# Kernel optimization log

Measured on AMD Instinct MI355X. Metric: run time of the kernel, lower is better.

Reference implementation:

```python
import jax, jax.numpy as jnp
import numpy as np

DIM = 1024
INTER = 4096
NUM_EXPERTS = 8
TOP_K = 2
NUM_TOKENS = 8192


def setup_inputs() -> dict:
    key = jax.random.key(0)
    ks = jax.random.split(key, 6)
    scale = 0.02
    return {
        "hidden_states": jax.random.normal(ks[0], (NUM_TOKENS, DIM), dtype=jnp.float32),
        # shared expert (stored as [in, out] so y = x @ W; same math as torch Linear)
        "shared_w1": jax.random.normal(ks[1], (DIM, INTER), dtype=jnp.float32) * scale,
        "shared_w2": jax.random.normal(ks[2], (INTER, DIM), dtype=jnp.float32) * scale,
        # routed experts, stacked: [E, in, out]
        "routed_w1": jax.random.normal(ks[3], (NUM_EXPERTS, DIM, INTER), dtype=jnp.float32) * scale,
        "routed_w2": jax.random.normal(ks[4], (NUM_EXPERTS, INTER, DIM), dtype=jnp.float32) * scale,
        # router: [dim, E]
        "router_w": jax.random.normal(ks[5], (DIM, NUM_EXPERTS), dtype=jnp.float32) * scale,
    }


def reference(hidden_states, shared_w1, shared_w2, routed_w1, routed_w2, router_w):
    # shared expert FFN
    shared_out = jnp.maximum(hidden_states @ shared_w1, 0) @ shared_w2  # [T, D]

    # router -> top-k -> softmax over the selected logits
    router_logits = hidden_states @ router_w                      # [T, E]
    top_vals, top_idx = jax.lax.top_k(router_logits, TOP_K)       # [T, K]
    routing_weights = jax.nn.softmax(top_vals, axis=-1)           # [T, K]

    # per-token combine weight for each expert: [T, E]
    onehot = jax.nn.one_hot(top_idx, NUM_EXPERTS, dtype=hidden_states.dtype)  # [T, K, E]
    combine = jnp.einsum('tk,tke->te', routing_weights, onehot)   # [T, E]

    # dense all-expert FFN (same math as gather/scatter loop, vectorized)
    h = jnp.einsum('td,edf->etf', hidden_states, routed_w1)       # [E, T, F]
    h = jnp.maximum(h, 0)
    expert_out = jnp.einsum('etf,efd->etd', h, routed_w2)         # [E, T, D]
    routed_out = jnp.einsum('etd,te->td', expert_out, combine)    # [T, D]

    return shared_out + routed_out
```

## Files before the change

### kernel.cpp

```cpp
#include <hip/hip_runtime.h>
#include <hip/hip_bf16.h>


#define T_TOKENS 8192
#define DIM      1024
#define INTER    4096
#define NEXP     8

typedef short bf16x8 __attribute__((ext_vector_type(8)));
typedef float f32x4  __attribute__((ext_vector_type(4)));

#define ASM_VMCNT(n) asm volatile("s_waitcnt vmcnt(" #n ")" ::: "memory")
#define ASM_BAR()    asm volatile("s_barrier" ::: "memory")

__device__ __forceinline__ unsigned short f2b(float f) {
  union { float f; unsigned int u; } v; v.f = f;
  unsigned int u = v.u;
  return (unsigned short)((u + 0x7FFFu + ((u >> 16) & 1u)) >> 16);
}

__device__ __forceinline__ void load_lds16(const unsigned short* g, unsigned short* l) {
  __builtin_amdgcn_global_load_lds(
      (const __attribute__((address_space(1))) void*)g,
      (__attribute__((address_space(3))) void*)l, 16, 0, 0);
}

__global__ void cast_x_kernel(const float* __restrict__ x, unsigned short* __restrict__ xb) {
  size_t i = ((size_t)blockIdx.x * 256 + threadIdx.x) * 4;
  float4 v = *(const float4*)(x + i);
  ushort4 o;
  o.x = f2b(v.x); o.y = f2b(v.y); o.z = f2b(v.z); o.w = f2b(v.w);
  *(ushort4*)(xb + i) = o;
}

__global__ void transpose_cast_kernel(const float* __restrict__ routed,
                                      const float* __restrict__ shared_w,
                                      unsigned short* __restrict__ outb,
                                      int K, int N) {
  int e = blockIdx.z;
  const float* in = (e < NEXP) ? routed + (size_t)e * K * N : shared_w;
  unsigned short* out = outb + (size_t)e * K * N;
  __shared__ float tile[32][33];
  int n0 = blockIdx.x * 32, k0 = blockIdx.y * 32;
  int tid = threadIdx.x;
  int c = tid & 31, r0 = tid >> 5;
#pragma unroll
  for (int i = 0; i < 4; i++) {
    int r = r0 + i * 8;
    tile[r][c] = in[(size_t)(k0 + r) * N + n0 + c];
  }
  __syncthreads();
  int rr = tid >> 3;
  int c4 = (tid & 7) * 4;
  ushort4 o;
  o.x = f2b(tile[c4 + 0][rr]); o.y = f2b(tile[c4 + 1][rr]);
  o.z = f2b(tile[c4 + 2][rr]); o.w = f2b(tile[c4 + 3][rr]);
  *(ushort4*)(out + (size_t)(n0 + rr) * K + k0 + c4) = o;
}

__global__ void router_topk_kernel(const float* __restrict__ x, const float* __restrict__ rw,
                                   int* __restrict__ top_idx, float* __restrict__ top_w) {
  int wv = threadIdx.x >> 6, lane = threadIdx.x & 63;
  int t = blockIdx.x * 4 + wv;
  const float* xr = x + (size_t)t * DIM;
  float a[8];
#pragma unroll
  for (int e = 0; e < 8; e++) a[e] = 0.f;
#pragma unroll
  for (int i = 0; i < 16; i++) {
    int d = i * 64 + lane;
    float xv = xr[d];
    float4 r0 = *(const float4*)(rw + d * 8);
    float4 r1 = *(const float4*)(rw + d * 8 + 4);
    a[0] += xv * r0.x; a[1] += xv * r0.y; a[2] += xv * r0.z; a[3] += xv * r0.w;
    a[4] += xv * r1.x; a[5] += xv * r1.y; a[6] += xv * r1.z; a[7] += xv * r1.w;
  }
#pragma unroll
  for (int s = 32; s; s >>= 1) {
#pragma unroll
    for (int e = 0; e < 8; e++) a[e] += __shfl_down(a[e], s);
  }
  if (lane == 0) {
    int be = 0; float bv = a[0];
#pragma unroll
    for (int e = 1; e < 8; e++) if (a[e] > bv) { bv = a[e]; be = e; }
    int be2 = -1; float bv2 = -3.4e38f;
#pragma unroll
    for (int e = 0; e < 8; e++) if (e != be && a[e] > bv2) { bv2 = a[e]; be2 = e; }
    float w0 = 1.f / (1.f + __expf(bv2 - bv));
    top_idx[t] = be | (be2 << 8);
    top_w[t] = w0;
  }
}

__global__ void bucket_kernel(const int* __restrict__ top_idx, const float* __restrict__ top_w,
                              int* __restrict__ counts, int* __restrict__ offs,
                              int* __restrict__ tok_list, float* __restrict__ tok_w) {
  __shared__ int lcount[NEXP];
  int tid = threadIdx.x;
  if (tid < NEXP) lcount[tid] = 0;
  __syncthreads();
  for (int t = tid; t < T_TOKENS; t += 256) {
    int p = top_idx[t];
    float w0 = top_w[t];
    int e0 = p & 0xff, e1 = p >> 8;
    int s0 = atomicAdd(&lcount[e0], 1);
    tok_list[e0 * T_TOKENS + s0] = t; tok_w[e0 * T_TOKENS + s0] = w0;
    int s1 = atomicAdd(&lcount[e1], 1);
    tok_list[e1 * T_TOKENS + s1] = t; tok_w[e1 * T_TOKENS + s1] = 1.f - w0;
  }
  __syncthreads();
  if (tid == 0) {
    int run = 0;
    for (int e = 0; e < NEXP; e++) { counts[e] = lcount[e]; offs[e] = run; run += lcount[e]; }
    offs[NEXP] = run;
  }
}

template <int PHASE>
__global__ __launch_bounds__(512, 2) void gemm_kernel(
    const unsigned short* __restrict__ A, const unsigned short* __restrict__ Wt,
    unsigned short* __restrict__ H, float* __restrict__ Out,
    const int* __restrict__ counts, const int* __restrict__ offs,
    const int* __restrict__ tok_list, const float* __restrict__ tok_w,
    int expert_arg, int accmode) {
  const int Kd = (PHASE == 1) ? DIM : INTER;
  int zz = (int)blockIdx.z;
  int expert, ksp;
  if (expert_arg >= 0) { expert = expert_arg; ksp = 0; }
  else if (PHASE == 2) { expert = zz % 9; ksp = zz / 9; }
  else { expert = zz; ksp = 0; }

  int count = (expert < NEXP) ? counts[expert] : T_TOKENS;
  int m0 = blockIdx.y * 256;
  if (m0 >= count) return;
  int n0 = blockIdx.x * 256;
  int hbase = (expert_arg >= 0) ? 0 : ((expert < NEXP) ? offs[expert] : 2 * T_TOKENS);
  const unsigned short* Bt = Wt + (size_t)expert * (4096 * 1024);

  int nt, k0base;
  if (PHASE == 1) { nt = 32; k0base = 0; }
  else if (expert_arg >= 0) { nt = 128; k0base = 0; }
  else { nt = 64; k0base = ksp * 2048; }

  __shared__ __align__(16) unsigned short As[4][256 * 32];
  __shared__ __align__(16) unsigned short Bs[4][256 * 32];

  int tid = threadIdx.x;
  int wv = tid >> 6, lane = tid & 63;
  int wv_m = wv >> 2, wv_n = wv & 3;
  int m_woff = wv_m * 128, n_woff = wv_n * 64;

  int g = (lane & 7) ^ (lane >> 3);
  int kc = (g & 3) * 8;
  const unsigned short* aG[2];
  const unsigned short* bG[2];
  int ldsOff[2];
#pragma unroll
  for (int j = 0; j < 2; j++) {
    int tr = j * 128 + wv * 16 + 2 * (lane >> 3) + (g >> 2);
    int srcA;
    if (PHASE == 1) {
      int m = m0 + tr;
      srcA = (expert < NEXP) ? ((m < count) ? tok_list[expert * T_TOKENS + m] : 0) : m;
    } else {
      srcA = hbase + m0 + tr;
    }
    aG[j] = A + (size_t)srcA * Kd + k0base + kc;
    bG[j] = Bt + (size_t)(n0 + tr) * Kd + k0base + kc;
    ldsOff[j] = j * 4096 + wv * 512;
  }

  f32x4 acc[8][4];
#pragma unroll
  for (int mf = 0; mf < 8; mf++)
#pragma unroll
    for (int nf = 0; nf < 4; nf++) acc[mf][nf] = (f32x4)0.f;

  int l15 = lane & 15, q = lane >> 4;
  int slot = (((l15 & 1) << 2) | q) ^ (l15 >> 1);
  int aBase = (wv_m * 64 + (l15 >> 1)) * 64 + slot * 8;
  int bBase = (wv_n * 32 + (l15 >> 1)) * 64 + slot * 8;

  auto stage = [&](int buf) {
#pragma unroll
    for (int j = 0; j < 2; j++) {
      load_lds16(aG[j], &As[buf][ldsOff[j]]);
      load_lds16(bG[j], &Bs[buf][ldsOff[j]]);
      aG[j] += 32; bG[j] += 32;
    }
  };

  auto compute_tile = [&](int buf) {
    const unsigned short* Ab = &As[buf][0];
    const unsigned short* Bb = &Bs[buf][0];
    bf16x8 af[8], bfr[4];
#pragma unroll
    for (int mf = 0; mf < 8; mf++) af[mf] = *(const bf16x8*)&Ab[aBase + mf * 512];
#pragma unroll
    for (int nf = 0; nf < 4; nf++) bfr[nf] = *(const bf16x8*)&Bb[bBase + nf * 512];
    __builtin_amdgcn_s_setprio(1);
#pragma unroll
    for (int mf = 0; mf < 8; mf++)
#pragma unroll
      for (int nf = 0; nf < 4; nf++)
        acc[mf][nf] = __builtin_amdgcn_mfma_f32_16x16x32_bf16(af[mf], bfr[nf], acc[mf][nf], 0, 0, 0);
    __builtin_amdgcn_s_setprio(0);
  };

  stage(0); stage(1); stage(2);
  ASM_VMCNT(8); ASM_BAR();
  int t = 0;
  for (; t + 3 < nt; ++t) {
    stage((t + 3) & 3);
    compute_tile(t & 3);
    ASM_VMCNT(8); ASM_BAR();
  }
  compute_tile(t & 3); ASM_VMCNT(4); ASM_BAR(); ++t;
  compute_tile(t & 3); ASM_VMCNT(0); ASM_BAR(); ++t;
  compute_tile(t & 3);

  if (PHASE == 1) {
#pragma unroll
    for (int mf = 0; mf < 8; mf++)
#pragma unroll
      for (int i = 0; i < 4; i++) {
        int m = m0 + m_woff + mf * 16 + q * 4 + i;
        if (m < count) {
#pragma unroll
          for (int nf = 0; nf < 4; nf++) {
            int f = n0 + n_woff + nf * 16 + l15;
            float v = acc[mf][nf][i];
            H[(size_t)(hbase + m) * INTER + f] = f2b(v > 0.f ? v : 0.f);
          }
        }
      }
  } else {
#pragma unroll
    for (int mf = 0; mf < 8; mf++)
#pragma unroll
      for (int i = 0; i < 4; i++) {
        int m = m0 + m_woff + mf * 16 + q * 4 + i;
        if (m < count) {
          int tokn; float swt;
          if (expert < NEXP) { tokn = tok_list[expert * T_TOKENS + m]; swt = tok_w[expert * T_TOKENS + m]; }
          else { tokn = m; swt = 1.f; }
          float* orow = Out + (size_t)tokn * DIM;
#pragma unroll
          for (int nf = 0; nf < 4; nf++) {
            int d = n0 + n_woff + nf * 16 + l15;
            float v = swt * acc[mf][nf][i];
            if (accmode) atomicAdd(orow + d, v);
            else if (expert < NEXP) orow[d] += v;
            else orow[d] = v;
          }
        }
      }
  }
}

extern "C" void kernel_launch(void* const* d_in, const int* in_sizes, int n_in,
                              void* d_out, int out_size, void* d_ws, size_t ws_size,
                              hipStream_t stream) {
  const float* x   = (const float*)d_in[0];
  const float* sw1 = (const float*)d_in[1];
  const float* sw2 = (const float*)d_in[2];
  const float* rw1 = (const float*)d_in[3];
  const float* rw2 = (const float*)d_in[4];
  const float* rtw = (const float*)d_in[5];
  float* out = (float*)d_out;

  char* ws = (char*)d_ws;
  unsigned short* xb  = (unsigned short*)(ws);
  unsigned short* w1t = (unsigned short*)(ws + 16777216);
  unsigned short* w2t = (unsigned short*)(ws + 92274688);
  unsigned short* h   = (unsigned short*)(ws + 167772160);
  int*   top_idx      = (int*)(ws + 167772160);
  float* top_w        = (float*)(ws + 167772160 + 32768);

  const size_t H_BIG  = (size_t)24576 * 4096 * 2;
  const size_t H_SMALL= (size_t)8192  * 4096 * 2;
  const size_t NEED_BIG = 167772160 + H_BIG + 262144 * 2 + 256;
  bool big = ws_size >= NEED_BIG;
  size_t tail = 167772160 + (big ? H_BIG : H_SMALL);
  int*   tok_list = (int*)(ws + tail);
  float* tok_w    = (float*)(ws + tail + 262144);
  int*   counts   = (int*)(ws + tail + 524288);
  int*   offs     = (int*)(ws + tail + 524288 + 64);

  cast_x_kernel<<<(T_TOKENS * DIM) / (256 * 4), 256, 0, stream>>>(x, xb);
  transpose_cast_kernel<<<dim3(128, 32, 9), 256, 0, stream>>>(rw1, sw1, w1t, 1024, 4096);
  transpose_cast_kernel<<<dim3(32, 128, 9), 256, 0, stream>>>(rw2, sw2, w2t, 4096, 1024);
  router_topk_kernel<<<T_TOKENS / 4, 256, 0, stream>>>(x, rtw, top_idx, top_w);
  bucket_kernel<<<1, 256, 0, stream>>>(top_idx, top_w, counts, offs, tok_list, tok_w);

  if (big) {
    hipMemsetAsync(out, 0, (size_t)T_TOKENS * DIM * sizeof(float), stream);
    gemm_kernel<1><<<dim3(16, 32, 9), 512, 0, stream>>>(xb, w1t, h, nullptr,
                                                        counts, offs, tok_list, tok_w, -1, 1);
    gemm_kernel<2><<<dim3(4, 32, 18), 512, 0, stream>>>(h, w2t, nullptr, out,
                                                        counts, offs, tok_list, tok_w, -1, 1);
  } else {
    gemm_kernel<1><<<dim3(16, 32), 512, 0, stream>>>(xb, w1t, h, nullptr,
                                                     counts, offs, tok_list, tok_w, 8, 0);
    gemm_kernel<2><<<dim3(4, 32), 512, 0, stream>>>(h, w2t, nullptr, out,
                                                    counts, offs, tok_list, tok_w, 8, 0);
    for (int e = 0; e < 8; e++) {
      gemm_kernel<1><<<dim3(16, 32), 512, 0, stream>>>(xb, w1t, h, nullptr,
                                                       counts, offs, tok_list, tok_w, e, 0);
      gemm_kernel<2><<<dim3(4, 32), 512, 0, stream>>>(h, w2t, nullptr, out,
                                                      counts, offs, tok_list, tok_w, e, 0);
    }
  }
}
```

Before: 1.172 ms.

## Split GEMM tile compute into two barrier-fenced phases interleaving LDS reads and staging

Restructures the inner GEMM loop so each K tile is computed in two halves. Each half first issues its LDS fragment reads and part of the global-to-LDS prefetch, then runs its block of MFMAs under raised priority, with s_barrier and lgkmcnt waits placed explicitly. The aim is to keep waves in lockstep so memory issue and matrix work from different waves overlap, in the style of a ping-pong schedule. It adds four barriers per tile, which may cost more than the overlap gains, and halves the number of A fragments held in registers at once.

New measurement: 1.069 ms. 8.8% less time.

```diff
diff --git a/kernel.cpp b/kernel.cpp
--- a/kernel.cpp
+++ b/kernel.cpp
@@ -11,6 +11,7 @@
 typedef float f32x4  __attribute__((ext_vector_type(4)));
 
 #define ASM_VMCNT(n) asm volatile("s_waitcnt vmcnt(" #n ")" ::: "memory")
+#define ASM_LGKM0()  asm volatile("s_waitcnt lgkmcnt(0)" ::: "memory")
 #define ASM_BAR()    asm volatile("s_barrier" ::: "memory")
 
 __device__ __forceinline__ unsigned short f2b(float f) {
@@ -182,6 +183,8 @@
   int aBase = (wv_m * 64 + (l15 >> 1)) * 64 + slot * 8;
   int bBase = (wv_n * 32 + (l15 >> 1)) * 64 + slot * 8;
 
+  bf16x8 af_lo[4], af_hi[4], bfr[4];
+
   auto stage = [&](int buf) {
 #pragma unroll
     for (int j = 0; j < 2; j++) {
@@ -191,34 +194,66 @@
     }
   };
 
-  auto compute_tile = [&](int buf) {
-    const unsigned short* Ab = &As[buf][0];
-    const unsigned short* Bb = &Bs[buf][0];
-    bf16x8 af[8], bfr[4];
-#pragma unroll
-    for (int mf = 0; mf < 8; mf++) af[mf] = *(const bf16x8*)&Ab[aBase + mf * 512];
-#pragma unroll
-    for (int nf = 0; nf < 4; nf++) bfr[nf] = *(const bf16x8*)&Bb[bBase + nf * 512];
+  auto phaseA = [&](int buf, int sbuf, bool doStage) {
+#pragma unroll
+    for (int mf = 0; mf < 4; mf++) af_lo[mf] = *(const bf16x8*)&As[buf][aBase + mf * 512];
+#pragma unroll
+    for (int nf = 0; nf < 4; nf++) bfr[nf]  = *(const bf16x8*)&Bs[buf][bBase + nf * 512];
+    if (doStage) {
+      load_lds16(aG[0], &As[sbuf][ldsOff[0]]);
+      load_lds16(bG[0], &Bs[sbuf][ldsOff[0]]);
+      aG[0] += 32; bG[0] += 32;
+    }
+    ASM_BAR();
+    ASM_LGKM0();
+    __builtin_amdgcn_sched_barrier(0);
     __builtin_amdgcn_s_setprio(1);
 #pragma unroll
-    for (int mf = 0; mf < 8; mf++)
+    for (int mf = 0; mf < 4; mf++)
 #pragma unroll
       for (int nf = 0; nf < 4; nf++)
-        acc[mf][nf] = __builtin_amdgcn_mfma_f32_16x16x32_bf16(af[mf], bfr[nf], acc[mf][nf], 0, 0, 0);
+        acc[mf][nf] = __builtin_amdgcn_mfma_f32_16x16x32_bf16(af_lo[mf], bfr[nf], acc[mf][nf], 0, 0, 0);
     __builtin_amdgcn_s_setprio(0);
+    ASM_BAR();
+  };
+
+  auto phaseB_pre = [&](int buf, int sbuf, bool doStage) {
+#pragma unroll
+    for (int mf = 0; mf < 4; mf++) af_hi[mf] = *(const bf16x8*)&As[buf][aBase + 2048 + mf * 512];
+    if (doStage) {
+      load_lds16(aG[1], &As[sbuf][ldsOff[1]]);
+      load_lds16(bG[1], &Bs[sbuf][ldsOff[1]]);
+      aG[1] += 32; bG[1] += 32;
+    }
+  };
+
+  auto phaseB_post = [&]() {
+    ASM_BAR();
+    ASM_LGKM0();
+    __builtin_amdgcn_sched_barrier(0);
+    __builtin_amdgcn_s_setprio(1);
+#pragma unroll
+    for (int mf = 0; mf < 4; mf++)
+#pragma unroll
+      for (int nf = 0; nf < 4; nf++)
+        acc[4 + mf][nf] = __builtin_amdgcn_mfma_f32_16x16x32_bf16(af_hi[mf], bfr[nf], acc[4 + mf][nf], 0, 0, 0);
+    __builtin_amdgcn_s_setprio(0);
+    ASM_BAR();
   };
 
   stage(0); stage(1); stage(2);
   ASM_VMCNT(8); ASM_BAR();
   int t = 0;
   for (; t + 3 < nt; ++t) {
-    stage((t + 3) & 3);
-    compute_tile(t & 3);
-    ASM_VMCNT(8); ASM_BAR();
-  }
-  compute_tile(t & 3); ASM_VMCNT(4); ASM_BAR(); ++t;
-  compute_tile(t & 3); ASM_VMCNT(0); ASM_BAR(); ++t;
-  compute_tile(t & 3);
+    int buf = t & 3, sbuf = (t + 3) & 3;
+    phaseA(buf, sbuf, true);
+    phaseB_pre(buf, sbuf, true);
+    ASM_VMCNT(8);
+    phaseB_post();
+  }
+  phaseA(t & 3, 0, false); phaseB_pre(t & 3, 0, false); ASM_VMCNT(4); phaseB_post(); ++t;
+  phaseA(t & 3, 0, false); phaseB_pre(t & 3, 0, false); ASM_VMCNT(0); phaseB_post(); ++t;
+  phaseA(t & 3, 0, false); phaseB_pre(t & 3, 0, false); phaseB_post();
 
   if (PHASE == 1) {
 #pragma unroll
```
